# Optimization experiments

Measured on AMD Instinct MI355X. Metric: run time of the kernel, lower is better.

Reference implementation:

```python
import jax, jax.numpy as jnp
import numpy as np

N_EDGE_TYPES = 25
EF = 2  # edge feature dim (excluding type)
HID = 10


def _edge_nn(et, ef, emb, wh, bh, wg, bg):
    # y = relu(emb[et] * (ef@Wh+bh) + (ef@Wg+bg)) -> [E, in*out]
    return jax.nn.relu(emb[et] * (ef @ wh + bh) + (ef @ wg + bg))


def _nnconv(x, et, ef, src, dst, emb, wh, bh, wg, bg, root, bias, in_c, out_c):
    n = x.shape[0]
    w = _edge_nn(et, ef, emb, wh, bh, wg, bg).reshape(-1, in_c, out_c)  # [E,in,out]
    msg = jnp.einsum('ei,eio->eo', x[src], w)                          # per-edge matmul
    s = jax.ops.segment_sum(msg, dst, num_segments=n)
    cnt = jax.ops.segment_sum(jnp.ones((src.shape[0],), x.dtype), dst, num_segments=n)
    agg = s / jnp.maximum(cnt, 1.0)[:, None]                           # scatter-mean
    return agg + x @ root + bias


def _make_params(key, in_c, out_c):
    ks = jax.random.split(key, 6)
    d = in_c * out_c
    s = 0.1
    return dict(
        emb=jax.random.normal(ks[0], (N_EDGE_TYPES, d), jnp.float32) * s,
        wh=jax.random.normal(ks[1], (EF, d), jnp.float32) * s,
        bh=jax.random.normal(ks[2], (d,), jnp.float32) * s,
        wg=jax.random.normal(ks[3], (EF, d), jnp.float32) * s,
        bg=jax.random.normal(ks[4], (d,), jnp.float32) * s,
        root=jax.random.normal(ks[5], (in_c, out_c), jnp.float32) * s,
        bias=jnp.zeros((out_c,), jnp.float32),
    )


def setup_inputs() -> dict:
    key = jax.random.key(0)
    ks = jax.random.split(key, 12)
    N, E, IN_C, OUT_C, B = 50000, 250000, 16, 16, 8
    inp = {
        'x': jax.random.normal(ks[0], (N, IN_C), jnp.float32),
        'edge_feat': jax.random.normal(ks[1], (E, EF), jnp.float32),
        'edge_type': jax.random.randint(ks[2], (E,), 0, N_EDGE_TYPES),
        'edge_src': jax.random.randint(ks[3], (E,), 0, N),
        'edge_dst': jax.random.randint(ks[4], (E,), 0, N),
        'cell_type': jax.random.randint(ks[5], (N,), 0, 3),
        'batch_ids': jnp.sort(jax.random.randint(ks[6], (N,), 0, B)),
        'batch_size': B,
    }
    for i, (ic, oc) in enumerate([(IN_C, HID), (HID, HID), (HID, OUT_C)], start=1):
        p = _make_params(ks[6 + i], ic, oc)
        for k, v in p.items():
            inp[f'{k}{i}'] = v
    return inp


def reference(x, edge_feat,
              emb1, wh1, bh1, wg1, bg1, root1, bias1,
              emb2, wh2, bh2, wg2, bg2, root2, bias2,
              emb3, wh3, bh3, wg3, bg3, root3, bias3,
              edge_type, edge_src, edge_dst, cell_type, batch_ids, batch_size):
    in_c, out_c = x.shape[1], root3.shape[1]
    h = _nnconv(x, edge_type, edge_feat, edge_src, edge_dst,
                emb1, wh1, bh1, wg1, bg1, root1, bias1, in_c, HID)
    h = jax.nn.relu(h)  # dropout is identity in eval mode
    h = _nnconv(h, edge_type, edge_feat, edge_src, edge_dst,
                emb2, wh2, bh2, wg2, bg2, root2, bias2, HID, HID)
    h = jax.nn.relu(h)
    h = _nnconv(h, edge_type, edge_feat, edge_src, edge_dst,
                emb3, wh3, bh3, wg3, bg3, root3, bias3, HID, out_c)
    h = jax.nn.relu(h)
    # scatter-mean pooling over nodes with cell_type==1, grouped by graph id
    gate = (cell_type == 1).astype(jnp.int32)
    idx = gate * (batch_ids.astype(jnp.int32) + 1)  # 0 = discarded bucket
    nseg = batch_size + 1
    s = jax.ops.segment_sum(h, idx, num_segments=nseg)
    cnt = jax.ops.segment_sum(jnp.ones((h.shape[0],), h.dtype), idx, num_segments=nseg)
    pooled = s / jnp.maximum(cnt, 1.0)[:, None]
    return pooled[1:batch_size + 1, :]  # [B, out_c]
```

## Files before the change

### kernel.cpp

```cpp
#include <hip/hip_runtime.h>
#include <stdint.h>

#define IN1 16
#define HIDC 10
#define OUT3 16
#define NTYPES 25
#define MAXB 32
#define XSTR 16

__global__ __launch_bounds__(256) void zero2_kernel(int* __restrict__ a, int na,
                                                    int* __restrict__ b, int nb) {
  int i = blockIdx.x * blockDim.x + threadIdx.x;
  int s = gridDim.x * blockDim.x;
  for (int j = i; j < na; j += s) a[j] = 0;
  for (int j = i; j < nb; j += s) b[j] = 0;
}

__global__ __launch_bounds__(256) void hist_kernel(const int* __restrict__ edst,
                                                   int* __restrict__ deg,
                                                   int* __restrict__ pos, int E) {
  int e = blockIdx.x * blockDim.x + threadIdx.x;
  if (e < E) pos[e] = atomicAdd(&deg[edst[e]], 1);
}

__global__ __launch_bounds__(1024) void scan_kernel(const int4* __restrict__ deg4,
                                                    int* __restrict__ row_ptr, int N) {
  __shared__ int wsums[16];
  __shared__ int s_run;
  int tid = threadIdx.x, lane = tid & 63, wid = tid >> 6;
  if (tid == 0) s_run = 0;
  __syncthreads();
  int N4 = (N + 3) >> 2;
  for (int base = 0; base < N4; base += 1024) {
    int i4 = base + tid;
    int4 v = make_int4(0, 0, 0, 0);
    if (i4 < N4) v = deg4[i4];
    int idx0 = i4 * 4;
    if (idx0 + 1 >= N) v.y = 0;
    if (idx0 + 2 >= N) v.z = 0;
    if (idx0 + 3 >= N) v.w = 0;
    int s = v.x + v.y + v.z + v.w;
    int x = s;
    #pragma unroll
    for (int off = 1; off < 64; off <<= 1) {
      int y = __shfl_up(x, off);
      if (lane >= off) x += y;
    }
    if (lane == 63) wsums[wid] = x;
    __syncthreads();
    if (tid < 16) {
      int w = wsums[tid];
      #pragma unroll
      for (int off = 1; off < 16; off <<= 1) {
        int y = __shfl_up(w, off);
        if (tid >= off) w += y;
      }
      wsums[tid] = w;
    }
    __syncthreads();
    int excl = x - s + ((wid > 0) ? wsums[wid - 1] : 0) + s_run;
    int total = wsums[15];
    if (idx0 < N) row_ptr[idx0] = excl;
    if (idx0 + 1 < N) row_ptr[idx0 + 1] = excl + v.x;
    if (idx0 + 2 < N) row_ptr[idx0 + 2] = excl + v.x + v.y;
    if (idx0 + 3 < N) row_ptr[idx0 + 3] = excl + v.x + v.y + v.z;
    __syncthreads();
    if (tid == 0) s_run += total;
    __syncthreads();
  }
  if (threadIdx.x == 0) row_ptr[N] = s_run;
}

__global__ __launch_bounds__(256) void permute_kernel(
    const int* __restrict__ edst, const int* __restrict__ esrc,
    const int* __restrict__ et, const float2* __restrict__ ef,
    const int* __restrict__ row_ptr, const int* __restrict__ pos,
    int4* __restrict__ edges, int E) {
  int e = blockIdx.x * blockDim.x + threadIdx.x;
  if (e >= E) return;
  int d = edst[e];
  int idx = row_ptr[d] + pos[e];
  float2 f = ef[e];
  int4 r;
  r.x = esrc[e];
  r.y = et[e];
  r.z = __float_as_int(f.x);
  r.w = __float_as_int(f.y);
  edges[idx] = r;
}

template<int IN_C, int O, bool POOL, int BS>
__global__ __launch_bounds__(BS) void layer_kernel(
    const float* __restrict__ xin,
    const int4* __restrict__ edges,
    const int* __restrict__ row_ptr,
    const float* __restrict__ emb,
    const float* __restrict__ wh, const float* __restrict__ bh,
    const float* __restrict__ wg, const float* __restrict__ bg,
    const float* __restrict__ root,
    const float* __restrict__ bias,
    float* __restrict__ hout,
    const int* __restrict__ ctype, const int* __restrict__ bids,
    float* __restrict__ pcnt,
    int N, int B)
{
  constexpr int D = IN_C * O;
  constexpr int ESTR = D + 8;
  constexpr int NPB = BS / 16;
  constexpr int XQ = (IN_C + 3) / 4;
  __shared__ float4 s_pa[D];
  __shared__ float2 s_pb[D];
  __shared__ float s_emb[NTYPES * ESTR];
  __shared__ float s_root[D];
  __shared__ float s_bias[O];
  __shared__ float s_psum[POOL ? (MAXB * 16) : 1];
  __shared__ float s_pcnt[POOL ? MAXB : 1];

  int tid = threadIdx.x;
  for (int k = tid; k < D; k += BS) {
    s_pa[k] = make_float4(wh[k], wh[D + k], wg[k], wg[D + k]);
    s_pb[k] = make_float2(bh[k], bg[k]);
    s_root[k] = root[k];
  }
  for (int k = tid; k < NTYPES * D; k += BS) {
    int t = k / D, j = k - t * D;
    s_emb[t * ESTR + j] = emb[k];
  }
  if (tid < O) s_bias[tid] = bias[tid];
  if (POOL) {
    for (int i = tid; i < MAXB * 16; i += BS) s_psum[i] = 0.f;
    for (int i = tid; i < MAXB; i += BS) s_pcnt[i] = 0.f;
  }
  __syncthreads();

  int nl = tid >> 4;
  int o = tid & 15;
  int oc = (O == 16) ? o : ((o < O) ? o : 0);
  int n = blockIdx.x * NPB + nl;

  float acc0 = 0.f, acc1 = 0.f;
  int start = 0, end = 0;
  if (n < N) { start = row_ptr[n]; end = row_ptr[n + 1]; }
  int nE = end - start;
  const int4* __restrict__ ep = edges + start;

  float xa[4 * XQ], xb[4 * XQ];
  int4 rA = make_int4(0, 0, 0, 0), rB = make_int4(0, 0, 0, 0);

  auto loadx = [&](float* xd, int src) {
    const float4* __restrict__ p = (const float4*)(xin + (size_t)src * XSTR);
    #pragma unroll
    for (int q = 0; q < XQ; ++q) {
      float4 v = p[q];
      xd[4 * q + 0] = v.x; xd[4 * q + 1] = v.y;
      xd[4 * q + 2] = v.z; xd[4 * q + 3] = v.w;
    }
  };
  auto edge_compute = [&](const int4& r, const float* xd) {
    int t = r.y;
    float f0 = __int_as_float(r.z), f1 = __int_as_float(r.w);
    const float* __restrict__ er = s_emb + t * ESTR;
    #pragma unroll
    for (int i = 0; i < IN_C; ++i) {
      int k = i * O + oc;
      float4 a = s_pa[k];
      float2 b = s_pb[k];
      float h = fmaf(f0, a.x, fmaf(f1, a.y, b.x));
      float g = fmaf(f0, a.z, fmaf(f1, a.w, b.y));
      float w = fmaxf(fmaf(er[k], h, g), 0.f);
      if (i & 1) acc1 = fmaf(xd[i], w, acc1);
      else       acc0 = fmaf(xd[i], w, acc0);
    }
  };

  if (nE > 0) {
    rA = ep[0];
    if (nE > 1) rB = ep[1];
    loadx(xa, rA.x);
    if (nE > 1) loadx(xb, rB.x);
    int j = 0;
    while (true) {
      {
        bool pf = (j + 2 < nE);
        int4 rn = make_int4(0, 0, 0, 0);
        if (pf) rn = ep[j + 2];
        edge_compute(rA, xa);
        if (pf) { rA = rn; loadx(xa, rA.x); }
      }
      if (++j >= nE) break;
      {
        bool pf = (j + 2 < nE);
        int4 rn = make_int4(0, 0, 0, 0);
        if (pf) rn = ep[j + 2];
        edge_compute(rB, xb);
        if (pf) { rB = rn; loadx(xb, rB.x); }
      }
      if (++j >= nE) break;
    }
  }

  float acc = acc0 + acc1;

  if (n < N && o < O) {
    float inv = 1.0f / fmaxf((float)nE, 1.0f);
    float v = fmaf(acc, inv, s_bias[o]);
    const float* __restrict__ xr = xin + (size_t)n * XSTR;
    #pragma unroll
    for (int i = 0; i < IN_C; ++i) v = fmaf(xr[i], s_root[i * O + o], v);
    v = fmaxf(v, 0.f);
    if (!POOL) {
      hout[(size_t)n * XSTR + o] = v;
    } else {
      if (ctype[n] == 1) {
        int b = bids[n];
        atomicAdd(&s_psum[b * 16 + o], v);
        if (o == 0) atomicAdd(&s_pcnt[b], 1.0f);
      }
    }
  }

  if (POOL) {
    __syncthreads();
    for (int i = tid; i < B * 16; i += BS) {
      float v = s_psum[i];
      if (v != 0.f) atomicAdd(&hout[i], v);
    }
    for (int i = tid; i < B; i += BS) {
      float c = s_pcnt[i];
      if (c != 0.f) atomicAdd(&pcnt[i], c);
    }
  }
}

__global__ __launch_bounds__(256) void finalize_kernel(
    const float* __restrict__ psum, const float* __restrict__ pcnt,
    float* __restrict__ out, int B) {
  int i = blockIdx.x * blockDim.x + threadIdx.x;
  if (i >= B * OUT3) return;
  int b = i / OUT3;
  out[i] = psum[i] / fmaxf(pcnt[b], 1.0f);
}

extern "C" void kernel_launch(void* const* d_in, const int* in_sizes, int n_in,
                              void* d_out, int out_size, void* d_ws, size_t ws_size,
                              hipStream_t stream)
{
  const float* x     = (const float*)d_in[0];
  const float* ef    = (const float*)d_in[1];
  const int*   et    = (const int*)d_in[2];
  const int*   esrc  = (const int*)d_in[3];
  const int*   edst  = (const int*)d_in[4];
  const int*   ctype = (const int*)d_in[5];
  const int*   bids  = (const int*)d_in[6];
  const float* emb1 = (const float*)d_in[8];
  const float* wh1  = (const float*)d_in[9];
  const float* bh1  = (const float*)d_in[10];
  const float* wg1  = (const float*)d_in[11];
  const float* bg1  = (const float*)d_in[12];
  const float* root1= (const float*)d_in[13];
  const float* bias1= (const float*)d_in[14];
  const float* emb2 = (const float*)d_in[15];
  const float* wh2  = (const float*)d_in[16];
  const float* bh2  = (const float*)d_in[17];
  const float* wg2  = (const float*)d_in[18];
  const float* bg2  = (const float*)d_in[19];
  const float* root2= (const float*)d_in[20];
  const float* bias2= (const float*)d_in[21];
  const float* emb3 = (const float*)d_in[22];
  const float* wh3  = (const float*)d_in[23];
  const float* bh3  = (const float*)d_in[24];
  const float* wg3  = (const float*)d_in[25];
  const float* bg3  = (const float*)d_in[26];
  const float* root3= (const float*)d_in[27];
  const float* bias3= (const float*)d_in[28];

  const int N = in_sizes[0] / IN1;
  const int E = in_sizes[2];
  const int B = out_size / OUT3;

  int4* edges   = (int4*)d_ws;
  int*  deg     = (int*)(edges + E);
  int*  pos     = deg + N;
  int*  row_ptr = pos + E;
  float* h1 = (float*)((((uintptr_t)(row_ptr + (N + 1))) + 15) & ~(uintptr_t)15);
  float* h2     = h1 + (size_t)N * XSTR;
  float* psum   = h2 + (size_t)N * XSTR;
  float* pcnt   = psum + (size_t)B * 16;

  zero2_kernel<<<128, 256, 0, stream>>>(deg, N, (int*)psum, B * 16 + B);
  hist_kernel<<<(E + 255) / 256, 256, 0, stream>>>(edst, deg, pos, E);
  scan_kernel<<<1, 1024, 0, stream>>>((const int4*)deg, row_ptr, N);
  permute_kernel<<<(E + 255) / 256, 256, 0, stream>>>(
      edst, esrc, et, (const float2*)ef, row_ptr, pos, edges, E);

  const int g256 = (N + 15) / 16;
  layer_kernel<IN1, HIDC, false, 256><<<g256, 256, 0, stream>>>(
      x, edges, row_ptr, emb1, wh1, bh1, wg1, bg1, root1, bias1,
      h1, nullptr, nullptr, nullptr, N, B);
  layer_kernel<HIDC, HIDC, false, 256><<<g256, 256, 0, stream>>>(
      h1, edges, row_ptr, emb2, wh2, bh2, wg2, bg2, root2, bias2,
      h2, nullptr, nullptr, nullptr, N, B);

  const int g1024 = (N + 63) / 64;
  layer_kernel<HIDC, OUT3, true, 1024><<<g1024, 1024, 0, stream>>>(
      h2, edges, row_ptr, emb3, wh3, bh3, wg3, bg3, root3, bias3,
      psum, ctype, bids, pcnt, N, B);

  finalize_kernel<<<1, 256, 0, stream>>>(psum, pcnt, (float*)d_out, B);
}
```

Before: 299.0 us.

## Hold edge-net weights in registers and split layer-1 input dim across two lane groups

Per-thread edge-network weights (wh, wg, bh, bg columns) now sit in registers instead of being read from shared memory for every edge. Layer 1 splits its 16 input channels across two 16-lane groups per node, combined with a shuffle-xor, which doubles the threads per node and halves the per-thread inner loop. The aim is fewer LDS loads per edge and more parallelism in the widest layer. In exchange, register pressure rises and every layer-1 edge record is fetched by twice as many lanes.

```diff
diff --git a/kernel.cpp b/kernel.cpp
--- a/kernel.cpp
+++ b/kernel.cpp
@@ -89,7 +89,7 @@
   edges[idx] = r;
 }
 
-template<int IN_C, int O, bool POOL, int BS>
+template<int IN_C, int O, int ISPLIT, bool POOL, int BS>
 __global__ __launch_bounds__(BS) void layer_kernel(
     const float* __restrict__ xin,
     const int4* __restrict__ edges,
@@ -105,11 +105,10 @@
     int N, int B)
 {
   constexpr int D = IN_C * O;
-  constexpr int ESTR = D + 8;
-  constexpr int NPB = BS / 16;
-  constexpr int XQ = (IN_C + 3) / 4;
-  __shared__ float4 s_pa[D];
-  __shared__ float2 s_pb[D];
+  constexpr int ESTR = D + 16;
+  constexpr int G = 16 * ISPLIT;
+  constexpr int NPB = BS / G;
+  constexpr int IH = IN_C / ISPLIT;
   __shared__ float s_emb[NTYPES * ESTR];
   __shared__ float s_root[D];
   __shared__ float s_bias[O];
@@ -117,15 +116,11 @@
   __shared__ float s_pcnt[POOL ? MAXB : 1];
 
   int tid = threadIdx.x;
-  for (int k = tid; k < D; k += BS) {
-    s_pa[k] = make_float4(wh[k], wh[D + k], wg[k], wg[D + k]);
-    s_pb[k] = make_float2(bh[k], bg[k]);
-    s_root[k] = root[k];
-  }
   for (int k = tid; k < NTYPES * D; k += BS) {
     int t = k / D, j = k - t * D;
     s_emb[t * ESTR + j] = emb[k];
   }
+  for (int k = tid; k < D; k += BS) s_root[k] = root[k];
   if (tid < O) s_bias[tid] = bias[tid];
   if (POOL) {
     for (int i = tid; i < MAXB * 16; i += BS) s_psum[i] = 0.f;
@@ -133,10 +128,22 @@
   }
   __syncthreads();
 
-  int nl = tid >> 4;
-  int o = tid & 15;
+  int lg = tid & (G - 1);
+  int o = lg & 15;
+  int ihalf = lg >> 4;
+  int nl = tid / G;
+  int n = blockIdx.x * NPB + nl;
   int oc = (O == 16) ? o : ((o < O) ? o : 0);
-  int n = blockIdx.x * NPB + nl;
+  int i0 = ihalf * IH;
+  int kbase = i0 * O + oc;
+
+  float cwh0[IH], cwh1[IH], cbh[IH], cwg0[IH], cwg1[IH], cbg[IH];
+  #pragma unroll
+  for (int s = 0; s < IH; ++s) {
+    int k = kbase + s * O;
+    cwh0[s] = wh[k]; cwh1[s] = wh[D + k]; cbh[s] = bh[k];
+    cwg0[s] = wg[k]; cwg1[s] = wg[D + k]; cbg[s] = bg[k];
+  }
 
   float acc0 = 0.f, acc1 = 0.f;
   int start = 0, end = 0;
@@ -144,32 +151,36 @@
   int nE = end - start;
   const int4* __restrict__ ep = edges + start;
 
-  float xa[4 * XQ], xb[4 * XQ];
+  float xa[IH], xb[IH];
   int4 rA = make_int4(0, 0, 0, 0), rB = make_int4(0, 0, 0, 0);
 
   auto loadx = [&](float* xd, int src) {
-    const float4* __restrict__ p = (const float4*)(xin + (size_t)src * XSTR);
-    #pragma unroll
-    for (int q = 0; q < XQ; ++q) {
-      float4 v = p[q];
-      xd[4 * q + 0] = v.x; xd[4 * q + 1] = v.y;
-      xd[4 * q + 2] = v.z; xd[4 * q + 3] = v.w;
+    const float* __restrict__ p = xin + (size_t)src * XSTR + i0;
+    if constexpr (IH == 8) {
+      float4 v0 = ((const float4*)p)[0];
+      float4 v1 = ((const float4*)p)[1];
+      xd[0] = v0.x; xd[1] = v0.y; xd[2] = v0.z; xd[3] = v0.w;
+      xd[4] = v1.x; xd[5] = v1.y; xd[6] = v1.z; xd[7] = v1.w;
+    } else {
+      float4 v0 = ((const float4*)p)[0];
+      float4 v1 = ((const float4*)p)[1];
+      float2 v2 = ((const float2*)p)[4];
+      xd[0] = v0.x; xd[1] = v0.y; xd[2] = v0.z; xd[3] = v0.w;
+      xd[4] = v1.x; xd[5] = v1.y; xd[6] = v1.z; xd[7] = v1.w;
+      xd[8] = v2.x; xd[9] = v2.y;
     }
   };
   auto edge_compute = [&](const int4& r, const float* xd) {
     int t = r.y;
     float f0 = __int_as_float(r.z), f1 = __int_as_float(r.w);
-    const float* __restrict__ er = s_emb + t * ESTR;
+    const float* __restrict__ er = s_emb + t * ESTR + kbase;
     #pragma unroll
-    for (int i = 0; i < IN_C; ++i) {
-      int k = i * O + oc;
-      float4 a = s_pa[k];
-      float2 b = s_pb[k];
-      float h = fmaf(f0, a.x, fmaf(f1, a.y, b.x));
-      float g = fmaf(f0, a.z, fmaf(f1, a.w, b.y));
-      float w = fmaxf(fmaf(er[k], h, g), 0.f);
-      if (i & 1) acc1 = fmaf(xd[i], w, acc1);
-      else       acc0 = fmaf(xd[i], w, acc0);
+    for (int s = 0; s < IH; ++s) {
+      float h = fmaf(f0, cwh0[s], fmaf(f1, cwh1[s], cbh[s]));
+      float g = fmaf(f0, cwg0[s], fmaf(f1, cwg1[s], cbg[s]));
+      float w = fmaxf(fmaf(er[s * O], h, g), 0.f);
+      if (s & 1) acc1 = fmaf(xd[s], w, acc1);
+      else       acc0 = fmaf(xd[s], w, acc0);
     }
   };
 
@@ -200,8 +211,9 @@
   }
 
   float acc = acc0 + acc1;
-
-  if (n < N && o < O) {
+  if constexpr (ISPLIT == 2) acc += __shfl_xor(acc, 16);
+
+  if (n < N && ihalf == 0 && o < O) {
     float inv = 1.0f / fmaxf((float)nE, 1.0f);
     float v = fmaf(acc, inv, s_bias[o]);
     const float* __restrict__ xr = xin + (size_t)n * XSTR;
@@ -293,16 +305,16 @@
   permute_kernel<<<(E + 255) / 256, 256, 0, stream>>>(
       edst, esrc, et, (const float2*)ef, row_ptr, pos, edges, E);
 
-  const int g256 = (N + 15) / 16;
-  layer_kernel<IN1, HIDC, false, 256><<<g256, 256, 0, stream>>>(
+  const int g1 = (N + 7) / 8;
+  layer_kernel<IN1, HIDC, 2, false, 256><<<g1, 256, 0, stream>>>(
       x, edges, row_ptr, emb1, wh1, bh1, wg1, bg1, root1, bias1,
       h1, nullptr, nullptr, nullptr, N, B);
-  layer_kernel<HIDC, HIDC, false, 256><<<g256, 256, 0, stream>>>(
+  const int g2 = (N + 15) / 16;
+  layer_kernel<HIDC, HIDC, 1, false, 256><<<g2, 256, 0, stream>>>(
       h1, edges, row_ptr, emb2, wh2, bh2, wg2, bg2, root2, bias2,
       h2, nullptr, nullptr, nullptr, N, B);
-
-  const int g1024 = (N + 63) / 64;
-  layer_kernel<HIDC, OUT3, true, 1024><<<g1024, 1024, 0, stream>>>(
+  const int g3 = (N + 63) / 64;
+  layer_kernel<HIDC, OUT3, 1, true, 1024><<<g3, 1024, 0, stream>>>(
       h2, edges, row_ptr, emb3, wh3, bh3, wg3, bg3, root3, bias3,
       psum, ctype, bids, pcnt, N, B);
 
```

Result: slower. 336.1 us (+12.4%).
